# Optimization experiments

Measured on AMD Instinct MI355X. Metric: run time of the kernel, lower is better.

The kernel has to match this reference:

```python
import jax, jax.numpy as jnp
import numpy as np

B, T, D, H = 2, 2048, 1024, 16
HD = D // H  # 64


def setup_inputs() -> dict:
    key = jax.random.key(0)
    ks = jax.random.split(key, 9)
    s = 1.0 / np.sqrt(D)
    return {
        "x": jax.random.normal(ks[0], (B, T, D), dtype=jnp.float32),
        "Wq": jax.random.uniform(ks[1], (D, D), minval=-s, maxval=s, dtype=jnp.float32),
        "bq": jax.random.uniform(ks[2], (D,), minval=-s, maxval=s, dtype=jnp.float32),
        "Wk": jax.random.uniform(ks[3], (D, D), minval=-s, maxval=s, dtype=jnp.float32),
        "bk": jax.random.uniform(ks[4], (D,), minval=-s, maxval=s, dtype=jnp.float32),
        "Wv": jax.random.uniform(ks[5], (D, D), minval=-s, maxval=s, dtype=jnp.float32),
        "bv": jax.random.uniform(ks[6], (D,), minval=-s, maxval=s, dtype=jnp.float32),
        "Wo": jax.random.uniform(ks[7], (D, D), minval=-s, maxval=s, dtype=jnp.float32),
        "bo": jax.random.uniform(ks[8], (D,), minval=-s, maxval=s, dtype=jnp.float32),
    }


def reference(x, Wq, bq, Wk, bk, Wv, bv, Wo, bo):
    b, t, d = x.shape
    # projections (nn.Linear: x @ W.T + b), split heads -> [B,H,T,hd]
    def split_heads(y):
        return y.reshape(b, t, H, HD).transpose(0, 2, 1, 3)
    Q = split_heads(x @ Wq.T + bq)
    K = split_heads(x @ Wk.T + bk)
    V = split_heads(x @ Wv.T + bv)
    # causal linear attention via cumulative outer-product state
    # Z[b,h,s,p,n] = V[b,h,s,p] * K[b,h,s,n]
    Z = jnp.einsum('bhsp,bhsn->bhspn', V, K)
    Z_cum = jnp.cumsum(Z, axis=2)  # prefix sum over time -> causal state
    Y = jnp.einsum('bhtn,bhtpn->bhtp', Q, Z_cum)  # [B,H,T,hd]
    Y = Y.transpose(0, 2, 1, 3).reshape(b, t, d)
    return Y @ Wo.T + bo
```

## Files before the change

kernel.cpp:

```cpp
#include <hip/hip_runtime.h>
#include <stdint.h>

#define B_  2
#define T_  2048
#define D_  1024
#define H_  16
#define HD_ 64
#define M_  (B_*T_)
#define CHK 128
#define NC  (T_/CHK)
#define BH  (B_*H_)

#define XN   4194304
#define WN   1048576

typedef unsigned short ushort_t;
typedef unsigned int   uint_t;

typedef __bf16 bf16x8 __attribute__((ext_vector_type(8)));
typedef float  f32x4  __attribute__((ext_vector_type(4)));

__device__ inline ushort_t f2bf(float f) {
    uint_t x = __float_as_uint(f);
    x += 0x7fffu + ((x >> 16) & 1u);
    return (ushort_t)(x >> 16);
}
__device__ inline float lo_bf(uint_t u) { return __uint_as_float(u << 16); }
__device__ inline float hi_bf(uint_t u) { return __uint_as_float(u & 0xffff0000u); }

__device__ inline uint4 pack8(const float4& lo, const float4& hi) {
    uint4 pk;
    pk.x = (uint_t)f2bf(lo.x) | ((uint_t)f2bf(lo.y) << 16);
    pk.y = (uint_t)f2bf(lo.z) | ((uint_t)f2bf(lo.w) << 16);
    pk.z = (uint_t)f2bf(hi.x) | ((uint_t)f2bf(hi.y) << 16);
    pk.w = (uint_t)f2bf(hi.z) | ((uint_t)f2bf(hi.w) << 16);
    return pk;
}

__global__ __launch_bounds__(256) void to_bf16_all(
    const float* __restrict__ x,  const float* __restrict__ Wq,
    const float* __restrict__ Wk, const float* __restrict__ Wv,
    const float* __restrict__ Wo, ushort_t* __restrict__ dst)
{
    const int idx = blockIdx.x * 256 + threadIdx.x;
    const int e   = idx * 8;
    const float* src;
    if      (e < XN)          src = x  + e;
    else if (e < XN + WN)     src = Wq + (e - XN);
    else if (e < XN + 2*WN)   src = Wk + (e - XN - WN);
    else if (e < XN + 3*WN)   src = Wv + (e - XN - 2*WN);
    else                      src = Wo + (e - XN - 3*WN);
    float4 lo = ((const float4*)src)[0];
    float4 hi = ((const float4*)src)[1];
    *(uint4*)(dst + e) = pack8(lo, hi);
}

__device__ inline void stage32(const ushort_t* __restrict__ g, ushort_t* ldsw, int lane) {
    const int rr  = lane >> 3;
    const int kg8 = ((lane & 7) ^ rr) << 3;
    const ushort_t* src = g + (size_t)rr * D_ + kg8;
    #pragma unroll
    for (int i = 0; i < 4; i++) {
        __builtin_amdgcn_global_load_lds(
            (const __attribute__((address_space(1))) void*)(src + (size_t)(i * 8) * D_),
            (__attribute__((address_space(3))) void*)(ldsw + i * 512),
            16, 0, 0);
    }
}

__global__ __launch_bounds__(256) void gemm_qkv(
    const ushort_t* __restrict__ xb, const ushort_t* __restrict__ Wqkvb,
    const float* __restrict__ bq, const float* __restrict__ bk,
    const float* __restrict__ bv, ushort_t* __restrict__ qkv_ws)
{
    const int z = blockIdx.z;
    const ushort_t* W  = Wqkvb + (size_t)z * WN;
    const float*    bi = (z == 0) ? bq : ((z == 1) ? bk : bv);
    ushort_t* out = qkv_ws + (size_t)z * (size_t)M_ * D_;

    __shared__ __align__(16) ushort_t As[128 * 64];
    __shared__ __align__(16) ushort_t Bs[128 * 64];

    const int tid  = threadIdx.x;
    const int m0   = blockIdx.y * 128;
    const int n0   = blockIdx.x * 128;
    const int wave = tid >> 6;
    const int lane = tid & 63;
    const int wm   = (wave >> 1) * 64;
    const int wn   = (wave & 1) * 64;
    const int fr   = lane & 15;
    const int quad = lane >> 4;

    const ushort_t* Ag = xb + (size_t)(m0 + wave * 32) * D_;
    const ushort_t* Bg = W  + (size_t)(n0 + wave * 32) * D_;
    ushort_t* Alds = &As[wave * 32 * 64];
    ushort_t* Blds = &Bs[wave * 32 * 64];

    f32x4 acc[4][4];
    #pragma unroll
    for (int i = 0; i < 4; i++)
        #pragma unroll
        for (int j = 0; j < 4; j++)
            acc[i][j] = (f32x4){0.f, 0.f, 0.f, 0.f};

    for (int k0 = 0; k0 < D_; k0 += 64) {
        __syncthreads();
        stage32(Ag + k0, Alds, lane);
        stage32(Bg + k0, Blds, lane);
        __syncthreads();

        #pragma unroll
        for (int ksg = 0; ksg <= 4; ksg += 4) {
            const int kgo = ((ksg + quad) ^ (fr & 7)) << 3;
            bf16x8 af[4], bf[4];
            #pragma unroll
            for (int i = 0; i < 4; i++) {
                uint4 u = *(const uint4*)&As[(wm + i * 16 + fr) * 64 + kgo];
                af[i] = __builtin_bit_cast(bf16x8, u);
            }
            #pragma unroll
            for (int j = 0; j < 4; j++) {
                uint4 u = *(const uint4*)&Bs[(wn + j * 16 + fr) * 64 + kgo];
                bf[j] = __builtin_bit_cast(bf16x8, u);
            }
            #pragma unroll
            for (int i = 0; i < 4; i++)
                #pragma unroll
                for (int j = 0; j < 4; j++)
                    acc[i][j] = __builtin_amdgcn_mfma_f32_16x16x32_bf16(
                        af[i], bf[j], acc[i][j], 0, 0, 0);
        }
    }

    const int rb = quad * 4;
    #pragma unroll
    for (int j = 0; j < 4; j++) {
        const int n = n0 + wn + j * 16 + fr;
        const float bias = bi[n];
        const int h  = n >> 6;
        const int hd = n & 63;
        #pragma unroll
        for (int i = 0; i < 4; i++) {
            #pragma unroll
            for (int r = 0; r < 4; r++) {
                const int m = m0 + wm + i * 16 + rb + r;
                const int b = m >> 11, t = m & (T_ - 1);
                out[(((size_t)(b * H_ + h)) * T_ + t) * HD_ + hd] =
                    f2bf(acc[i][j][r] + bias);
            }
        }
    }
}

__global__ __launch_bounds__(256) void gemm_out(
    const ushort_t* __restrict__ Yw, const ushort_t* __restrict__ Wob,
    const float* __restrict__ bo, float* __restrict__ out)
{
    __shared__ __align__(16) ushort_t As[128 * 64];
    __shared__ __align__(16) ushort_t Bs[128 * 64];

    const int tid  = threadIdx.x;
    const int m0   = blockIdx.y * 128;
    const int n0   = blockIdx.x * 128;
    const int wave = tid >> 6;
    const int lane = tid & 63;
    const int wm   = (wave >> 1) * 64;
    const int wn   = (wave & 1) * 64;
    const int fr   = lane & 15;
    const int quad = lane >> 4;

    const ushort_t* Ag = Yw  + (size_t)(m0 + wave * 32) * D_;
    const ushort_t* Bg = Wob + (size_t)(n0 + wave * 32) * D_;
    ushort_t* Alds = &As[wave * 32 * 64];
    ushort_t* Blds = &Bs[wave * 32 * 64];

    f32x4 acc[4][4];
    #pragma unroll
    for (int i = 0; i < 4; i++)
        #pragma unroll
        for (int j = 0; j < 4; j++)
            acc[i][j] = (f32x4){0.f, 0.f, 0.f, 0.f};

    for (int k0 = 0; k0 < D_; k0 += 64) {
        __syncthreads();
        stage32(Ag + k0, Alds, lane);
        stage32(Bg + k0, Blds, lane);
        __syncthreads();

        #pragma unroll
        for (int ksg = 0; ksg <= 4; ksg += 4) {
            const int kgo = ((ksg + quad) ^ (fr & 7)) << 3;
            bf16x8 af[4], bf[4];
            #pragma unroll
            for (int i = 0; i < 4; i++) {
                uint4 u = *(const uint4*)&As[(wm + i * 16 + fr) * 64 + kgo];
                af[i] = __builtin_bit_cast(bf16x8, u);
            }
            #pragma unroll
            for (int j = 0; j < 4; j++) {
                uint4 u = *(const uint4*)&Bs[(wn + j * 16 + fr) * 64 + kgo];
                bf[j] = __builtin_bit_cast(bf16x8, u);
            }
            #pragma unroll
            for (int i = 0; i < 4; i++)
                #pragma unroll
                for (int j = 0; j < 4; j++)
                    acc[i][j] = __builtin_amdgcn_mfma_f32_16x16x32_bf16(
                        af[i], bf[j], acc[i][j], 0, 0, 0);
        }
    }

    const int rb = quad * 4;
    #pragma unroll
    for (int j = 0; j < 4; j++) {
        const int n = n0 + wn + j * 16 + fr;
        const float bias = bo[n];
        #pragma unroll
        for (int i = 0; i < 4; i++) {
            #pragma unroll
            for (int r = 0; r < 4; r++) {
                const int m = m0 + wm + i * 16 + rb + r;
                out[(size_t)m * D_ + n] = acc[i][j][r] + bias;
            }
        }
    }
}

__global__ __launch_bounds__(256) void chunk_delta(
    const ushort_t* __restrict__ k_ws, const ushort_t* __restrict__ v_ws,
    float* __restrict__ deltas)
{
    const int c = blockIdx.x, bh = blockIdx.y;
    __shared__ __align__(16) ushort_t Ks[CHK * HD_];
    __shared__ __align__(16) ushort_t Vs[CHK * HD_];
    const int tid = threadIdx.x;
    const size_t base = ((size_t)bh * T_ + (size_t)c * CHK) * HD_;

    #pragma unroll
    for (int g = 0; g < 4; g++) {
        ((uint4*)Ks)[tid + 256 * g] = ((const uint4*)(k_ws + base))[tid + 256 * g];
        ((uint4*)Vs)[tid + 256 * g] = ((const uint4*)(v_ws + base))[tid + 256 * g];
    }
    __syncthreads();

    const int n  = tid & 63;
    const int pb = (tid >> 6) * 16;
    float acc[16];
    #pragma unroll
    for (int j = 0; j < 16; j++) acc[j] = 0.f;

    for (int s = 0; s < CHK; s++) {
        const float kv = lo_bf((uint_t)Ks[s * 64 + n]);
        uint4 u0 = *(const uint4*)&Vs[s * 64 + pb];
        uint4 u1 = *(const uint4*)&Vs[s * 64 + pb + 8];
        acc[0]  += kv * lo_bf(u0.x); acc[1]  += kv * hi_bf(u0.x);
        acc[2]  += kv * lo_bf(u0.y); acc[3]  += kv * hi_bf(u0.y);
        acc[4]  += kv * lo_bf(u0.z); acc[5]  += kv * hi_bf(u0.z);
        acc[6]  += kv * lo_bf(u0.w); acc[7]  += kv * hi_bf(u0.w);
        acc[8]  += kv * lo_bf(u1.x); acc[9]  += kv * hi_bf(u1.x);
        acc[10] += kv * lo_bf(u1.y); acc[11] += kv * hi_bf(u1.y);
        acc[12] += kv * lo_bf(u1.z); acc[13] += kv * hi_bf(u1.z);
        acc[14] += kv * lo_bf(u1.w); acc[15] += kv * hi_bf(u1.w);
    }

    float* dp = deltas + ((size_t)bh * NC + c) * 4096;
    #pragma unroll
    for (int j = 0; j < 16; j++) dp[(pb + j) * 64 + n] = acc[j];
}

__global__ __launch_bounds__(256) void prefix_states(
    const float* __restrict__ deltas, ushort_t* __restrict__ states_bf)
{
    const int bh = blockIdx.x, tid = threadIdx.x;
    float acc[16];
    #pragma unroll
    for (int j = 0; j < 16; j++) acc[j] = 0.f;
    for (int c = 0; c < NC; c++) {
        const float* dp = deltas    + ((size_t)bh * NC + c) * 4096;
        ushort_t*    sp = states_bf + ((size_t)bh * NC + c) * 4096;
        #pragma unroll
        for (int j = 0; j < 16; j++) {
            const int e = j * 256 + tid;
            sp[e] = f2bf(acc[j]);
            acc[j] += dp[e];
        }
    }
}

#define LDS_ 136
__global__ __launch_bounds__(256) void attn_chunk(
    const ushort_t* __restrict__ q_ws, const ushort_t* __restrict__ k_ws,
    const ushort_t* __restrict__ v_ws, const ushort_t* __restrict__ states_bf,
    ushort_t* __restrict__ y_ws)
{
    const int c = blockIdx.x, bh = blockIdx.y;
    __shared__ __align__(16) ushort_t VtS[64 * LDS_];
    __shared__ __align__(16) ushort_t Smat[128 * LDS_];

    const int tid  = threadIdx.x;
    const int wave = tid >> 6;
    const int lane = tid & 63;
    const int fr   = lane & 15;
    const int quad = lane >> 4;
    const int fk   = quad * 8;
    const int rb   = quad * 4;

    const size_t base = ((size_t)bh * T_ + (size_t)c * CHK) * HD_;
    const ushort_t* qg = q_ws + base;
    const ushort_t* kg = k_ws + base;
    const ushort_t* vg = v_ws + base;
    const ushort_t* st = states_bf + ((size_t)bh * NC + c) * 4096;

    #pragma unroll
    for (int g = 0; g < 4; g++) {
        const int v  = tid + 256 * g;
        const int s  = v >> 3;
        const int p8 = (v & 7) * 8;
        uint4 u = ((const uint4*)vg)[v];
        ushort_t e[8];
        *(uint4*)e = u;
        const int sb = s >> 3, slo = s & 7;
        #pragma unroll
        for (int j = 0; j < 8; j++) {
            const int p   = p8 + j;
            const int blk = (sb & 8) | ((sb ^ (p >> 3)) & 7);
            VtS[p * LDS_ + (blk << 3) + slo] = e[j];
        }
    }
    __syncthreads();

    const int mt[2] = { wave, 7 - wave };

    bf16x8 aq[2][2];
    #pragma unroll
    for (int i = 0; i < 2; i++)
        #pragma unroll
        for (int kk = 0; kk < 2; kk++) {
            uint4 u = *(const uint4*)(qg + (mt[i] * 16 + fr) * HD_ + kk * 32 + fk);
            aq[i][kk] = __builtin_bit_cast(bf16x8, u);
        }

    f32x4 acc[2][4];
    #pragma unroll
    for (int i = 0; i < 2; i++)
        #pragma unroll
        for (int jn = 0; jn < 4; jn++)
            acc[i][jn] = (f32x4){0.f, 0.f, 0.f, 0.f};

    #pragma unroll
    for (int jn = 0; jn < 4; jn++) {
        #pragma unroll
        for (int kk = 0; kk < 2; kk++) {
            uint4 u = *(const uint4*)(st + (jn * 16 + fr) * 64 + kk * 32 + fk);
            bf16x8 bsp = __builtin_bit_cast(bf16x8, u);
            #pragma unroll
            for (int i = 0; i < 2; i++)
                acc[i][jn] = __builtin_amdgcn_mfma_f32_16x16x32_bf16(
                    aq[i][kk], bsp, acc[i][jn], 0, 0, 0);
        }
    }

    #pragma unroll
    for (int i = 0; i < 2; i++) {
        const int m  = mt[i];
        const int nk = (m + 2) >> 1;
        const int jt = 2 * nk;

        f32x4 sc[8];
        #pragma unroll
        for (int j = 0; j < 8; j++) sc[j] = (f32x4){0.f, 0.f, 0.f, 0.f};

        #pragma unroll
        for (int j = 0; j < 8; j++) {
            if (j <= m) {
                #pragma unroll
                for (int kk = 0; kk < 2; kk++) {
                    uint4 u = *(const uint4*)(kg + (j * 16 + fr) * HD_ + kk * 32 + fk);
                    sc[j] = __builtin_amdgcn_mfma_f32_16x16x32_bf16(
                        aq[i][kk], __builtin_bit_cast(bf16x8, u), sc[j], 0, 0, 0);
                }
            }
        }

        #pragma unroll
        for (int j = 0; j < 8; j++) {
            if (j < jt) {
                f32x4 v = sc[j];
                if (j == m) {
                    #pragma unroll
                    for (int r = 0; r < 4; r++)
                        if (fr > rb + r) v[r] = 0.f;
                }
                #pragma unroll
                for (int r = 0; r < 4; r++)
                    Smat[(m * 16 + rb + r) * LDS_ + j * 16 + fr] = f2bf(v[r]);
            }
        }

        #pragma unroll
        for (int kt = 0; kt < 4; kt++) {
            if (kt < nk) {
                uint4 ua = *(const uint4*)&Smat[(m * 16 + fr) * LDS_ + kt * 32 + fk];
                bf16x8 as_ = __builtin_bit_cast(bf16x8, ua);
                #pragma unroll
                for (int jn = 0; jn < 4; jn++) {
                    const int p   = jn * 16 + fr;
                    const int sb  = kt * 4 + quad;
                    const int blk = (sb & 8) | ((sb ^ (p >> 3)) & 7);
                    uint4 ub = *(const uint4*)&VtS[p * LDS_ + (blk << 3)];
                    acc[i][jn] = __builtin_amdgcn_mfma_f32_16x16x32_bf16(
                        as_, __builtin_bit_cast(bf16x8, ub), acc[i][jn], 0, 0, 0);
                }
            }
        }
    }

    const int b = bh >> 4, h = bh & 15;
    ushort_t* yg = y_ws + ((size_t)(b * T_ + c * CHK)) * D_ + h * 64;
    #pragma unroll
    for (int i = 0; i < 2; i++) {
        #pragma unroll
        for (int jn = 0; jn < 4; jn++) {
            #pragma unroll
            for (int r = 0; r < 4; r++) {
                const int t = mt[i] * 16 + rb + r;
                const int p = jn * 16 + fr;
                yg[(size_t)t * D_ + p] = f2bf(acc[i][jn][r]);
            }
        }
    }
}

extern "C" void kernel_launch(void* const* d_in, const int* in_sizes, int n_in,
                              void* d_out, int out_size, void* d_ws, size_t ws_size,
                              hipStream_t stream)
{
    const float* x  = (const float*)d_in[0];
    const float* Wq = (const float*)d_in[1];
    const float* bq = (const float*)d_in[2];
    const float* Wk = (const float*)d_in[3];
    const float* bk = (const float*)d_in[4];
    const float* Wv = (const float*)d_in[5];
    const float* bv = (const float*)d_in[6];
    const float* Wo = (const float*)d_in[7];
    const float* bo = (const float*)d_in[8];
    float* out = (float*)d_out;

    ushort_t* cvt    = (ushort_t*)d_ws;
    ushort_t* xb     = cvt;
    ushort_t* Wqkvb  = cvt + (size_t)XN;
    ushort_t* Wob    = cvt + (size_t)XN + 3 * WN;
    ushort_t* q_ws   = cvt + (size_t)XN + 4 * WN;
    ushort_t* k_ws   = q_ws + (size_t)M_ * D_;
    ushort_t* v_ws   = k_ws + (size_t)M_ * D_;
    ushort_t* y_ws   = v_ws + (size_t)M_ * D_;
    float*    deltas    = (float*)xb;
    ushort_t* states_bf = Wqkvb;

    to_bf16_all<<<dim3((XN + 4 * WN) / 8 / 256), 256, 0, stream>>>(
        x, Wq, Wk, Wv, Wo, cvt);
    gemm_qkv<<<dim3(D_ / 128, M_ / 128, 3), 256, 0, stream>>>(
        xb, Wqkvb, bq, bk, bv, q_ws);
    chunk_delta<<<dim3(NC, BH), 256, 0, stream>>>(k_ws, v_ws, deltas);
    prefix_states<<<dim3(BH), 256, 0, stream>>>(deltas, states_bf);
    attn_chunk<<<dim3(NC, BH), 256, 0, stream>>>(q_ws, k_ws, v_ws, states_bf, y_ws);
    gemm_out<<<dim3(D_ / 128, M_ / 128), 256, 0, stream>>>(y_ws, Wob, bo, out);
}
```

Baseline: 201.3 us.

## Use MFMA for chunk deltas and fold prefix scan into attention kernel

Chunk delta computation (V^T K per chunk) now runs on bf16 MFMA instructions, with both K and V staged transposed into swizzled LDS, instead of scalar FMA loops. The separate serial prefix_states kernel is removed. Each attention block now sums the fp32 deltas of all earlier chunks itself while loading its state operand, which saves a launch and a low-parallelism serial kernel. The cost is redundant global reads that grow with chunk index, so later chunks sum up to 15 deltas.

```diff
diff --git a/kernel.cpp b/kernel.cpp
--- a/kernel.cpp
+++ b/kernel.cpp
@@ -34,6 +34,14 @@
     pk.y = (uint_t)f2bf(lo.z) | ((uint_t)f2bf(lo.w) << 16);
     pk.z = (uint_t)f2bf(hi.x) | ((uint_t)f2bf(hi.y) << 16);
     pk.w = (uint_t)f2bf(hi.z) | ((uint_t)f2bf(hi.w) << 16);
+    return pk;
+}
+__device__ inline uint4 pack8f(const f32x4& lo, const f32x4& hi) {
+    uint4 pk;
+    pk.x = (uint_t)f2bf(lo[0]) | ((uint_t)f2bf(lo[1]) << 16);
+    pk.y = (uint_t)f2bf(lo[2]) | ((uint_t)f2bf(lo[3]) << 16);
+    pk.z = (uint_t)f2bf(hi[0]) | ((uint_t)f2bf(hi[1]) << 16);
+    pk.w = (uint_t)f2bf(hi[2]) | ((uint_t)f2bf(hi[3]) << 16);
     return pk;
 }
 
@@ -226,71 +234,74 @@
     }
 }
 
+#define LDS_ 136
+
+__device__ inline void stage_T(const ushort_t* __restrict__ src, ushort_t* dst, int tid) {
+    #pragma unroll
+    for (int g = 0; g < 4; g++) {
+        const int v  = tid + 256 * g;
+        const int s  = v >> 3;
+        const int p8 = (v & 7) * 8;
+        uint4 u = ((const uint4*)src)[v];
+        ushort_t e[8];
+        *(uint4*)e = u;
+        const int sb = s >> 3, slo = s & 7;
+        #pragma unroll
+        for (int j = 0; j < 8; j++) {
+            const int p   = p8 + j;
+            const int blk = (sb & 8) | ((sb ^ (p >> 3)) & 7);
+            dst[p * LDS_ + (blk << 3) + slo] = e[j];
+        }
+    }
+}
+
 __global__ __launch_bounds__(256) void chunk_delta(
     const ushort_t* __restrict__ k_ws, const ushort_t* __restrict__ v_ws,
     float* __restrict__ deltas)
 {
     const int c = blockIdx.x, bh = blockIdx.y;
-    __shared__ __align__(16) ushort_t Ks[CHK * HD_];
-    __shared__ __align__(16) ushort_t Vs[CHK * HD_];
+    __shared__ __align__(16) ushort_t VtS[64 * LDS_];
+    __shared__ __align__(16) ushort_t KtS[64 * LDS_];
     const int tid = threadIdx.x;
+    const int wave = tid >> 6, lane = tid & 63;
+    const int fr = lane & 15, quad = lane >> 4, rb = quad * 4;
     const size_t base = ((size_t)bh * T_ + (size_t)c * CHK) * HD_;
 
-    #pragma unroll
-    for (int g = 0; g < 4; g++) {
-        ((uint4*)Ks)[tid + 256 * g] = ((const uint4*)(k_ws + base))[tid + 256 * g];
-        ((uint4*)Vs)[tid + 256 * g] = ((const uint4*)(v_ws + base))[tid + 256 * g];
-    }
+    stage_T(v_ws + base, VtS, tid);
+    stage_T(k_ws + base, KtS, tid);
     __syncthreads();
 
-    const int n  = tid & 63;
-    const int pb = (tid >> 6) * 16;
-    float acc[16];
-    #pragma unroll
-    for (int j = 0; j < 16; j++) acc[j] = 0.f;
-
-    for (int s = 0; s < CHK; s++) {
-        const float kv = lo_bf((uint_t)Ks[s * 64 + n]);
-        uint4 u0 = *(const uint4*)&Vs[s * 64 + pb];
-        uint4 u1 = *(const uint4*)&Vs[s * 64 + pb + 8];
-        acc[0]  += kv * lo_bf(u0.x); acc[1]  += kv * hi_bf(u0.x);
-        acc[2]  += kv * lo_bf(u0.y); acc[3]  += kv * hi_bf(u0.y);
-        acc[4]  += kv * lo_bf(u0.z); acc[5]  += kv * hi_bf(u0.z);
-        acc[6]  += kv * lo_bf(u0.w); acc[7]  += kv * hi_bf(u0.w);
-        acc[8]  += kv * lo_bf(u1.x); acc[9]  += kv * hi_bf(u1.x);
-        acc[10] += kv * lo_bf(u1.y); acc[11] += kv * hi_bf(u1.y);
-        acc[12] += kv * lo_bf(u1.z); acc[13] += kv * hi_bf(u1.z);
-        acc[14] += kv * lo_bf(u1.w); acc[15] += kv * hi_bf(u1.w);
+    const int p = wave * 16 + fr;
+    f32x4 acc[4];
+    #pragma unroll
+    for (int jn = 0; jn < 4; jn++) acc[jn] = (f32x4){0.f, 0.f, 0.f, 0.f};
+
+    #pragma unroll
+    for (int kt = 0; kt < 4; kt++) {
+        const int sb   = kt * 4 + quad;
+        const int blkA = (sb & 8) | ((sb ^ (p >> 3)) & 7);
+        bf16x8 af = __builtin_bit_cast(bf16x8, *(const uint4*)&VtS[p * LDS_ + (blkA << 3)]);
+        #pragma unroll
+        for (int jn = 0; jn < 4; jn++) {
+            const int n    = jn * 16 + fr;
+            const int blkB = (sb & 8) | ((sb ^ (n >> 3)) & 7);
+            uint4 ub = *(const uint4*)&KtS[n * LDS_ + (blkB << 3)];
+            acc[jn] = __builtin_amdgcn_mfma_f32_16x16x32_bf16(
+                af, __builtin_bit_cast(bf16x8, ub), acc[jn], 0, 0, 0);
+        }
     }
 
     float* dp = deltas + ((size_t)bh * NC + c) * 4096;
     #pragma unroll
-    for (int j = 0; j < 16; j++) dp[(pb + j) * 64 + n] = acc[j];
-}
-
-__global__ __launch_bounds__(256) void prefix_states(
-    const float* __restrict__ deltas, ushort_t* __restrict__ states_bf)
-{
-    const int bh = blockIdx.x, tid = threadIdx.x;
-    float acc[16];
-    #pragma unroll
-    for (int j = 0; j < 16; j++) acc[j] = 0.f;
-    for (int c = 0; c < NC; c++) {
-        const float* dp = deltas    + ((size_t)bh * NC + c) * 4096;
-        ushort_t*    sp = states_bf + ((size_t)bh * NC + c) * 4096;
-        #pragma unroll
-        for (int j = 0; j < 16; j++) {
-            const int e = j * 256 + tid;
-            sp[e] = f2bf(acc[j]);
-            acc[j] += dp[e];
-        }
-    }
-}
-
-#define LDS_ 136
+    for (int jn = 0; jn < 4; jn++)
+        #pragma unroll
+        for (int r = 0; r < 4; r++)
+            dp[(wave * 16 + rb + r) * 64 + jn * 16 + fr] = acc[jn][r];
+}
+
 __global__ __launch_bounds__(256) void attn_chunk(
     const ushort_t* __restrict__ q_ws, const ushort_t* __restrict__ k_ws,
-    const ushort_t* __restrict__ v_ws, const ushort_t* __restrict__ states_bf,
+    const ushort_t* __restrict__ v_ws, const float* __restrict__ deltas,
     ushort_t* __restrict__ y_ws)
 {
     const int c = blockIdx.x, bh = blockIdx.y;
@@ -309,24 +320,8 @@
     const ushort_t* qg = q_ws + base;
     const ushort_t* kg = k_ws + base;
     const ushort_t* vg = v_ws + base;
-    const ushort_t* st = states_bf + ((size_t)bh * NC + c) * 4096;
-
-    #pragma unroll
-    for (int g = 0; g < 4; g++) {
-        const int v  = tid + 256 * g;
-        const int s  = v >> 3;
-        const int p8 = (v & 7) * 8;
-        uint4 u = ((const uint4*)vg)[v];
-        ushort_t e[8];
-        *(uint4*)e = u;
-        const int sb = s >> 3, slo = s & 7;
-        #pragma unroll
-        for (int j = 0; j < 8; j++) {
-            const int p   = p8 + j;
-            const int blk = (sb & 8) | ((sb ^ (p >> 3)) & 7);
-            VtS[p * LDS_ + (blk << 3) + slo] = e[j];
-        }
-    }
+
+    stage_T(vg, VtS, tid);
     __syncthreads();
 
     const int mt[2] = { wave, 7 - wave };
@@ -351,8 +346,16 @@
     for (int jn = 0; jn < 4; jn++) {
         #pragma unroll
         for (int kk = 0; kk < 2; kk++) {
-            uint4 u = *(const uint4*)(st + (jn * 16 + fr) * 64 + kk * 32 + fk);
-            bf16x8 bsp = __builtin_bit_cast(bf16x8, u);
+            const int off = (jn * 16 + fr) * 64 + kk * 32 + fk;
+            const float* dp = deltas + (size_t)bh * NC * 4096 + off;
+            f32x4 lo = (f32x4){0.f, 0.f, 0.f, 0.f};
+            f32x4 hi = (f32x4){0.f, 0.f, 0.f, 0.f};
+            for (int cc = 0; cc < c; cc++) {
+                lo += ((const f32x4*)dp)[0];
+                hi += ((const f32x4*)dp)[1];
+                dp += 4096;
+            }
+            bf16x8 bsp = __builtin_bit_cast(bf16x8, pack8f(lo, hi));
             #pragma unroll
             for (int i = 0; i < 2; i++)
                 acc[i][jn] = __builtin_amdgcn_mfma_f32_16x16x32_bf16(
@@ -454,15 +457,13 @@
     ushort_t* k_ws   = q_ws + (size_t)M_ * D_;
     ushort_t* v_ws   = k_ws + (size_t)M_ * D_;
     ushort_t* y_ws   = v_ws + (size_t)M_ * D_;
-    float*    deltas    = (float*)xb;
-    ushort_t* states_bf = Wqkvb;
+    float*    deltas = (float*)xb;
 
     to_bf16_all<<<dim3((XN + 4 * WN) / 8 / 256), 256, 0, stream>>>(
         x, Wq, Wk, Wv, Wo, cvt);
     gemm_qkv<<<dim3(D_ / 128, M_ / 128, 3), 256, 0, stream>>>(
         xb, Wqkvb, bq, bk, bv, q_ws);
     chunk_delta<<<dim3(NC, BH), 256, 0, stream>>>(k_ws, v_ws, deltas);
-    prefix_states<<<dim3(BH), 256, 0, stream>>>(deltas, states_bf);
-    attn_chunk<<<dim3(NC, BH), 256, 0, stream>>>(q_ws, k_ws, v_ws, states_bf, y_ws);
+    attn_chunk<<<dim3(NC, BH), 256, 0, stream>>>(q_ws, k_ws, v_ws, deltas, y_ws);
     gemm_out<<<dim3(D_ / 128, M_ / 128), 256, 0, stream>>>(y_ws, Wob, bo, out);
 }
```

Result: slower. 236.8 us (+17.6%).
